# Kernel tuning notes

Measured on AMD Instinct MI355X. Metric: run time of the kernel, lower is better.

Reference implementation:

```python
import jax, jax.numpy as jnp
from jax import lax
import numpy as np

NPOINT = 1024
NSAMPLE = 32
BN_EPS = 1e-3  # Keras BatchNormalization default epsilon


def farthest_point_sample(xyz, npoint):
    # xyz: [B, N, 3] -> indices [B, npoint] (int32), sequential O(npoint*N)
    B, N, _ = xyz.shape

    def step(carry, _):
        distance, farthest = carry                                   # [B,N], [B]
        centroid = jnp.take_along_axis(xyz, farthest[:, None, None], axis=1)  # [B,1,3]
        dist = jnp.sum((xyz - centroid) ** 2, axis=-1)               # [B,N]
        distance = jnp.minimum(distance, dist)
        new_farthest = jnp.argmax(distance, axis=1).astype(jnp.int32)
        return (distance, new_farthest), farthest

    init = (jnp.full((B, N), 1e10, xyz.dtype), jnp.zeros((B,), jnp.int32))
    _, idxs = lax.scan(step, init, xs=None, length=npoint)           # [npoint, B]
    return jnp.transpose(idxs)                                       # [B, npoint]


def index_points_2d(points, idx):
    # points: [B,N,C], idx: [B,S] -> [B,S,C]
    return jnp.take_along_axis(points, idx[:, :, None], axis=1)


def index_points_3d(points, idx):
    # points: [B,N,C], idx: [B,S,K] -> [B,S,K,C]
    return jax.vmap(lambda p, i: p[i])(points, idx)


def query_ball_point(nsample, xyz, new_xyz):
    # nearest-nsample variant (radius is ignored, matching the source)
    # sq_dist: [B, S, N]
    sq = jnp.sum(new_xyz ** 2, axis=-1, keepdims=True) \
         - 2.0 * jnp.einsum('bsc,bnc->bsn', new_xyz, xyz) \
         + jnp.sum(xyz ** 2, axis=-1)[:, None, :]
    _, group_idx = lax.top_k(-sq, nsample)                           # [B,S,K]
    return group_idx


def bn_relu(x, g, b, mm, mv):
    # inference-mode BatchNorm (moving stats) + ReLU, per-channel on last dim
    return jax.nn.relu((x - mm) * lax.rsqrt(mv + BN_EPS) * g + b)


def setup_inputs() -> dict:
    key = jax.random.key(0)
    ks = jax.random.split(key, 20)
    B, N, D = 4, 16384, 64
    mlp = [64, 64, 128]
    cin = 3 + D  # 67
    inp = {
        'xyz': jax.random.normal(ks[0], (B, N, 3), jnp.float32),
        'points': jax.random.normal(ks[1], (B, N, D), jnp.float32),
    }
    c = cin
    for i, co in enumerate(mlp):
        inp[f'w{i}'] = jax.random.normal(ks[2 + 4 * i], (c, co), jnp.float32) * (1.0 / np.sqrt(c))
        inp[f'g{i}'] = jnp.ones((co,), jnp.float32)
        inp[f'b{i}'] = jnp.zeros((co,), jnp.float32)
        inp[f'mm{i}'] = jax.random.normal(ks[3 + 4 * i], (co,), jnp.float32) * 0.1
        inp[f'mv{i}'] = jax.random.uniform(ks[4 + 4 * i], (co,), jnp.float32, 0.5, 1.5)
        c = co
    return inp


def reference(xyz, points, w0, g0, b0, mm0, mv0, w1, g1, b1, mm1, mv1, w2, g2, b2, mm2, mv2):
    fps_idx = farthest_point_sample(xyz, NPOINT)                     # [B,S]
    new_xyz = index_points_2d(xyz, fps_idx)                          # [B,S,3]
    idx = query_ball_point(NSAMPLE, xyz, new_xyz)                    # [B,S,K]
    grouped_xyz = index_points_3d(xyz, idx)                          # [B,S,K,3]
    grouped_xyz_norm = grouped_xyz - new_xyz[:, :, None, :]
    grouped_points = index_points_3d(points, idx)                    # [B,S,K,D]
    x = jnp.concatenate([grouped_xyz_norm, grouped_points], axis=-1) # [B,S,K,3+D]
    for w, g, b, mm, mv in ((w0, g0, b0, mm0, mv0), (w1, g1, b1, mm1, mv1), (w2, g2, b2, mm2, mv2)):
        x = bn_relu(jnp.einsum('bskc,co->bsko', x, w), g, b, mm, mv)
    new_points = jnp.max(x, axis=2)                                  # [B,S,C_out]
    return (new_xyz, new_points)
```

## Files before the change

### kernel.cpp

```cpp
#include <hip/hip_runtime.h>
#include <hip/hip_bf16.h>
#include <stdint.h>

#define N_PTS 16384
#define S_OUT 1024


__global__ __launch_bounds__(512) void fps_kernel(
    const float* __restrict__ xyz,
    float* __restrict__ out_newxyz)
{
  const int b    = blockIdx.x;
  const int tid  = threadIdx.x;
  const int lane = tid & 63;
  const int wid  = tid >> 6;
  const float* base = xyz + (size_t)b * N_PTS * 3;

  float px[32], py[32], pz[32], dist[32];
#pragma unroll
  for (int i = 0; i < 32; ++i) {
    int n = tid * 32 + i;
    px[i] = base[n * 3 + 0];
    py[i] = base[n * 3 + 1];
    pz[i] = base[n * 3 + 2];
    dist[i] = 1e10f;
  }

  __shared__ float s_cx, s_cy, s_cz;
  __shared__ unsigned long long sred[8];

  if (tid == 0) { s_cx = px[0]; s_cy = py[0]; s_cz = pz[0]; }
  __syncthreads();

  for (int s = 0; s < S_OUT; ++s) {
    const float cx = s_cx, cy = s_cy, cz = s_cz;
    if (tid == 0) {
      size_t o = ((size_t)b * S_OUT + s) * 3;
      out_newxyz[o + 0] = cx;
      out_newxyz[o + 1] = cy;
      out_newxyz[o + 2] = cz;
    }
    unsigned long long best = 0ull;
#pragma unroll
    for (int i = 0; i < 32; ++i) {
      float dx = __fsub_rn(px[i], cx);
      float dy = __fsub_rn(py[i], cy);
      float dz = __fsub_rn(pz[i], cz);
      float dd = __fadd_rn(__fadd_rn(__fmul_rn(dx, dx), __fmul_rn(dy, dy)),
                           __fmul_rn(dz, dz));
      float dm = fminf(dist[i], dd);
      dist[i] = dm;
      unsigned long long key =
          ((unsigned long long)__float_as_uint(dm) << 32) |
          (unsigned long long)(0xFFFFFFFFu - (unsigned)(tid * 32 + i));
      if (key > best) best = key;
    }
#pragma unroll
    for (int off = 1; off < 64; off <<= 1) {
      unsigned long long o = __shfl_xor(best, off);
      if (o > best) best = o;
    }
    if (lane == 0) sred[wid] = best;
    __syncthreads();
    if (tid == 0) {
      unsigned long long m = sred[0];
#pragma unroll
      for (int w = 1; w < 8; ++w) if (sred[w] > m) m = sred[w];
      unsigned n = 0xFFFFFFFFu - (unsigned)(m & 0xFFFFFFFFull);
      const float* p = base + (size_t)n * 3;
      s_cx = p[0]; s_cy = p[1]; s_cz = p[2];
    }
    __syncthreads();
  }
}

__global__ __launch_bounds__(256, 2) void knn_kernel(
    const float* __restrict__ xyz,
    const float* __restrict__ newxyz,
    int* __restrict__ knn_out)
{
  const int bs  = blockIdx.x;
  const int b   = bs >> 10;
  const int tid = threadIdx.x;
  const float* base = xyz + (size_t)b * N_PTS * 3;

  const float qx = newxyz[(size_t)bs * 3 + 0];
  const float qy = newxyz[(size_t)bs * 3 + 1];
  const float qz = newxyz[(size_t)bs * 3 + 2];
  const float sumq = __fadd_rn(__fadd_rn(__fmul_rn(qx, qx), __fmul_rn(qy, qy)),
                               __fmul_rn(qz, qz));

  __shared__ unsigned hist[2048];
  __shared__ unsigned tsum[256];
  __shared__ unsigned long long cand[512];
  __shared__ unsigned long long s_min;
  __shared__ int s_b1, s_r1, s_b2, s_r2, s_cntL, s_cntC;

  for (int i = tid; i < 2048; i += 256) hist[i] = 0;
  if (tid == 0) { s_cntL = 0; s_cntC = 0; }
  __syncthreads();

#define KNN_KEY(n, u)                                                          \
    float x = base[(n) * 3 + 0];                                               \
    float y = base[(n) * 3 + 1];                                               \
    float z = base[(n) * 3 + 2];                                               \
    float sumx = __fadd_rn(__fadd_rn(__fmul_rn(x, x), __fmul_rn(y, y)),        \
                           __fmul_rn(z, z));                                   \
    float dot  = __fmul_rn(qx, x);                                             \
    dot = fmaf(qy, y, dot);                                                    \
    dot = fmaf(qz, z, dot);                                                    \
    float sq   = __fsub_rn(__fadd_rn(sumq, sumx), __fmul_rn(2.0f, dot));       \
    unsigned u = __float_as_uint(sq);                                          \
    u ^= (u & 0x80000000u) ? 0xFFFFFFFFu : 0x80000000u;

  for (int j = 0; j < 64; ++j) {
    int n = j * 256 + tid;
    KNN_KEY(n, u)
    atomicAdd(&hist[u >> 21], 1u);
  }
  __syncthreads();

  unsigned ts = 0;
#pragma unroll
  for (int u = 0; u < 8; ++u) ts += hist[tid * 8 + u];
  tsum[tid] = ts;
  __syncthreads();

  if (tid == 0) {
    unsigned acc = 0; int t2 = 0;
    for (; t2 < 256; ++t2) { unsigned h = tsum[t2]; if (acc + h >= 32u) break; acc += h; }
    int u2 = t2 * 8;
    for (;; ++u2) { unsigned h = hist[u2]; if (acc + h >= 32u) break; acc += h; }
    s_b1 = u2; s_r1 = 32 - (int)acc;
  }
  __syncthreads();
  const unsigned b1 = (unsigned)s_b1;
  const int r1 = s_r1;

  for (int i = tid; i < 2048; i += 256) hist[i] = 0;
  __syncthreads();

  for (int j = 0; j < 64; ++j) {
    int n = j * 256 + tid;
    KNN_KEY(n, u)
    if ((u >> 21) == b1) atomicAdd(&hist[(u >> 10) & 0x7FFu], 1u);
  }
  __syncthreads();

  ts = 0;
#pragma unroll
  for (int u = 0; u < 8; ++u) ts += hist[tid * 8 + u];
  tsum[tid] = ts;
  __syncthreads();

  if (tid == 0) {
    unsigned acc = 0; int t2 = 0;
    for (; t2 < 256; ++t2) { unsigned h = tsum[t2]; if (acc + h >= (unsigned)r1) break; acc += h; }
    int u2 = t2 * 8;
    for (;; ++u2) { unsigned h = hist[u2]; if (acc + h >= (unsigned)r1) break; acc += h; }
    s_b2 = u2; s_r2 = r1 - (int)acc;
  }
  __syncthreads();
  const unsigned b2 = (unsigned)s_b2;

  int* outp = knn_out + (size_t)bs * 32;

  for (int j = 0; j < 64; ++j) {
    int n = j * 256 + tid;
    KNN_KEY(n, u)
    unsigned bin = u >> 21;
    if (bin < b1) {
      int p = atomicAdd(&s_cntL, 1);
      outp[p] = n;
    } else if (bin == b1) {
      unsigned sub = (u >> 10) & 0x7FFu;
      if (sub < b2) {
        int p = atomicAdd(&s_cntL, 1);
        outp[p] = n;
      } else if (sub == b2) {
        int p = atomicAdd(&s_cntC, 1);
        if (p < 512) cand[p] = ((unsigned long long)u << 32) | (unsigned)n;
      }
    }
  }
  __syncthreads();
#undef KNN_KEY

  const int r   = s_r2;
  const int cl  = s_cntL;
  const int cnt = min(s_cntC, 512);
  unsigned long long last = 0ull;
  for (int i = 0; i < r; ++i) {
    if (tid == 0) s_min = ~0ull;
    __syncthreads();
    for (int p = tid; p < cnt; p += 256) {
      unsigned long long v = cand[p];
      if (i == 0 ? 1 : (v > last)) atomicMin(&s_min, v);
    }
    __syncthreads();
    unsigned long long m = s_min;
    if (tid == 0) outp[cl + i] = (int)(unsigned)(m & 0xFFFFFFFFull);
    last = m;
    __syncthreads();
  }
}

__global__ __launch_bounds__(256, 2) void mlp_kernel(
    const float* __restrict__ xyz,
    const float* __restrict__ points,
    const float* __restrict__ newxyz,
    const int* __restrict__ knn,
    const float* __restrict__ w0, const float* __restrict__ g0,
    const float* __restrict__ b0, const float* __restrict__ mm0,
    const float* __restrict__ mv0,
    const float* __restrict__ w1, const float* __restrict__ g1,
    const float* __restrict__ b1_, const float* __restrict__ mm1,
    const float* __restrict__ mv1,
    const float* __restrict__ w2, const float* __restrict__ g2,
    const float* __restrict__ b2_, const float* __restrict__ mm2,
    const float* __restrict__ mv2,
    float* __restrict__ out1)
{
  const int tid = threadIdx.x;
  const int BS0 = blockIdx.x * 2;

  __shared__ __align__(16) float xT[2][67][36];
  __shared__ __align__(16) float a1[2][64][36];
  __shared__ __align__(16) float wbuf[8192];

  {
    const int sg = tid >> 7;
    const int j  = (tid >> 2) & 31;
    const int cq = tid & 3;
    const int S  = BS0 + sg;
    const int bb = S >> 10;
    const int n  = knn[(size_t)S * 32 + j] & (N_PTS - 1);
    const float* pbase = points + ((size_t)bb * N_PTS + n) * 64;
    const float* xbase = xyz + ((size_t)bb * N_PTS + n) * 3;
    for (int c = cq; c < 67; c += 4) {
      float v;
      if (c < 3) v = __fsub_rn(xbase[c], newxyz[(size_t)S * 3 + c]);
      else       v = pbase[c - 3];
      xT[sg][c][j] = v;
    }
  }
  for (int i = tid; i < 67 * 64; i += 256) wbuf[i] = w0[i];
  __syncthreads();

  const int sg = tid >> 7;
  const int t  = tid & 127;

  {
    const int ot = t & 15, kt = t >> 4;
    const int o0 = ot * 4, k0 = kt * 4;
    float acc[4][4] = {};
    for (int c = 0; c < 67; ++c) {
      float4 xv = *(const float4*)&xT[sg][c][k0];
      float4 wq = *(const float4*)&wbuf[c * 64 + o0];
      float wv[4] = { wq.x, wq.y, wq.z, wq.w };
      float xs[4] = { xv.x, xv.y, xv.z, xv.w };
#pragma unroll
      for (int a = 0; a < 4; ++a)
#pragma unroll
        for (int k2 = 0; k2 < 4; ++k2)
          acc[a][k2] = fmaf(wv[a], xs[k2], acc[a][k2]);
    }
#pragma unroll
    for (int jj = 0; jj < 4; ++jj) {
      int o = o0 + jj;
      float A  = rsqrtf(mv0[o] + 1e-3f) * g0[o];
      float Bc = b0[o] - mm0[o] * A;
      float4 y;
      y.x = fmaxf(fmaf(acc[jj][0], A, Bc), 0.0f);
      y.y = fmaxf(fmaf(acc[jj][1], A, Bc), 0.0f);
      y.z = fmaxf(fmaf(acc[jj][2], A, Bc), 0.0f);
      y.w = fmaxf(fmaf(acc[jj][3], A, Bc), 0.0f);
      *(float4*)&a1[sg][o][k0] = y;
    }
  }
  __syncthreads();
  for (int i = tid; i < 64 * 64; i += 256) wbuf[i] = w1[i];
  __syncthreads();

  {
    const int ot = t & 15, kt = t >> 4;
    const int o0 = ot * 4, k0 = kt * 4;
    float acc[4][4] = {};
    for (int c = 0; c < 64; ++c) {
      float4 xv = *(const float4*)&a1[sg][c][k0];
      float4 wq = *(const float4*)&wbuf[c * 64 + o0];
      float wv[4] = { wq.x, wq.y, wq.z, wq.w };
      float xs[4] = { xv.x, xv.y, xv.z, xv.w };
#pragma unroll
      for (int a = 0; a < 4; ++a)
#pragma unroll
        for (int k2 = 0; k2 < 4; ++k2)
          acc[a][k2] = fmaf(wv[a], xs[k2], acc[a][k2]);
    }
#pragma unroll
    for (int jj = 0; jj < 4; ++jj) {
      int o = o0 + jj;
      float A  = rsqrtf(mv1[o] + 1e-3f) * g1[o];
      float Bc = b1_[o] - mm1[o] * A;
      float4 y;
      y.x = fmaxf(fmaf(acc[jj][0], A, Bc), 0.0f);
      y.y = fmaxf(fmaf(acc[jj][1], A, Bc), 0.0f);
      y.z = fmaxf(fmaf(acc[jj][2], A, Bc), 0.0f);
      y.w = fmaxf(fmaf(acc[jj][3], A, Bc), 0.0f);
      *(float4*)&xT[sg][o][k0] = y;
    }
  }
  __syncthreads();
  for (int i = tid; i < 64 * 128; i += 256) wbuf[i] = w2[i];
  __syncthreads();

  float* pm = &a1[0][0][0];
  {
    const int ot = t & 31, kt = t >> 5;
    const int o0 = ot * 4, k0 = kt * 8;
    float acc[4][8] = {};
    for (int c = 0; c < 64; ++c) {
      float4 xa = *(const float4*)&xT[sg][c][k0];
      float4 xb = *(const float4*)&xT[sg][c][k0 + 4];
      float4 wq = *(const float4*)&wbuf[c * 128 + o0];
      float wv[4] = { wq.x, wq.y, wq.z, wq.w };
      float xs[8] = { xa.x, xa.y, xa.z, xa.w, xb.x, xb.y, xb.z, xb.w };
#pragma unroll
      for (int a = 0; a < 4; ++a)
#pragma unroll
        for (int k2 = 0; k2 < 8; ++k2)
          acc[a][k2] = fmaf(wv[a], xs[k2], acc[a][k2]);
    }
#pragma unroll
    for (int jj = 0; jj < 4; ++jj) {
      int o = o0 + jj;
      float A  = rsqrtf(mv2[o] + 1e-3f) * g2[o];
      float Bc = b2_[o] - mm2[o] * A;
      float m = 0.0f;
#pragma unroll
      for (int kk = 0; kk < 8; ++kk)
        m = fmaxf(m, fmaf(acc[jj][kk], A, Bc));
      pm[((sg * 128 + o) << 2) + kt] = m;
    }
  }
  __syncthreads();
  {
    const int sg2 = tid >> 7, o = tid & 127;
    const int basep = (sg2 * 128 + o) << 2;
    float m = fmaxf(fmaxf(pm[basep + 0], pm[basep + 1]),
                    fmaxf(pm[basep + 2], pm[basep + 3]));
    out1[(size_t)(BS0 + sg2) * 128 + o] = m;
  }
}

extern "C" void kernel_launch(void* const* d_in, const int* in_sizes, int n_in,
                              void* d_out, int out_size, void* d_ws, size_t ws_size,
                              hipStream_t stream) {
  const float* xyz    = (const float*)d_in[0];
  const float* points = (const float*)d_in[1];
  const float* w0  = (const float*)d_in[2];
  const float* g0  = (const float*)d_in[3];
  const float* b0  = (const float*)d_in[4];
  const float* mm0 = (const float*)d_in[5];
  const float* mv0 = (const float*)d_in[6];
  const float* w1  = (const float*)d_in[7];
  const float* g1  = (const float*)d_in[8];
  const float* b1  = (const float*)d_in[9];
  const float* mm1 = (const float*)d_in[10];
  const float* mv1 = (const float*)d_in[11];
  const float* w2  = (const float*)d_in[12];
  const float* g2  = (const float*)d_in[13];
  const float* b2  = (const float*)d_in[14];
  const float* mm2 = (const float*)d_in[15];
  const float* mv2 = (const float*)d_in[16];

  float* out      = (float*)d_out;
  float* out_pts  = out + (size_t)4 * 1024 * 3;
  int*   knn      = (int*)d_ws;

  fps_kernel<<<4, 512, 0, stream>>>(xyz, out);
  knn_kernel<<<4096, 256, 0, stream>>>(xyz, out, knn);
  mlp_kernel<<<2048, 256, 0, stream>>>(xyz, points, out, knn,
      w0, g0, b0, mm0, mv0, w1, g1, b1, mm1, mv1, w2, g2, b2, mm2, mv2,
      out_pts);
}
```

Before: 2.099 ms.

## Streamline FPS argmax reduction with float shuffles and one barrier per step

The per-point argmax now keeps a float max plus a local index instead of building 64-bit keys. The wavefront reduction shuffles only the 32-bit float, then uses a ballot to find the winning lane's index. A double-buffered shared array lets every thread reduce the 8 per-wave results itself, which removes the second __syncthreads and the serial thread-0 centroid load per iteration. Launch bounds also request 2 blocks per CU. The cost is a redundant global load of the centroid by every thread, plus extra register pressure from the occupancy hint, which could cause spills of the 128 per-thread registers.

```diff
diff --git a/kernel.cpp b/kernel.cpp
--- a/kernel.cpp
+++ b/kernel.cpp
@@ -6,7 +6,7 @@
 #define S_OUT 1024
 
 
-__global__ __launch_bounds__(512) void fps_kernel(
+__global__ __launch_bounds__(512, 2) void fps_kernel(
     const float* __restrict__ xyz,
     float* __restrict__ out_newxyz)
 {
@@ -26,21 +26,21 @@
     dist[i] = 1e10f;
   }
 
-  __shared__ float s_cx, s_cy, s_cz;
-  __shared__ unsigned long long sred[8];
-
-  if (tid == 0) { s_cx = px[0]; s_cy = py[0]; s_cz = pz[0]; }
-  __syncthreads();
+  __shared__ unsigned long long sred[2][8];
+
+  float cx = base[0], cy = base[1], cz = base[2];
 
   for (int s = 0; s < S_OUT; ++s) {
-    const float cx = s_cx, cy = s_cy, cz = s_cz;
     if (tid == 0) {
       size_t o = ((size_t)b * S_OUT + s) * 3;
       out_newxyz[o + 0] = cx;
       out_newxyz[o + 1] = cy;
       out_newxyz[o + 2] = cz;
     }
-    unsigned long long best = 0ull;
+    if (s == S_OUT - 1) break;
+
+    float best  = -1.0f;
+    int   bestI = 0;
 #pragma unroll
     for (int i = 0; i < 32; ++i) {
       float dx = __fsub_rn(px[i], cx);
@@ -50,27 +50,36 @@
                            __fmul_rn(dz, dz));
       float dm = fminf(dist[i], dd);
       dist[i] = dm;
-      unsigned long long key =
-          ((unsigned long long)__float_as_uint(dm) << 32) |
-          (unsigned long long)(0xFFFFFFFFu - (unsigned)(tid * 32 + i));
-      if (key > best) best = key;
-    }
-#pragma unroll
-    for (int off = 1; off < 64; off <<= 1) {
-      unsigned long long o = __shfl_xor(best, off);
-      if (o > best) best = o;
-    }
-    if (lane == 0) sred[wid] = best;
+      bool c = dm > best;
+      best  = c ? dm : best;
+      bestI = c ? i  : bestI;
+    }
+    const unsigned bestN = (unsigned)(tid * 32 + bestI);
+
+    float m = best;
+#pragma unroll
+    for (int off = 1; off < 64; off <<= 1)
+      m = fmaxf(m, __shfl_xor(m, off));
+    unsigned long long msk = __ballot(best == m);
+    int wl = __ffsll(msk) - 1;
+    unsigned wn = (unsigned)__shfl((int)bestN, wl);
+
+    const int p = s & 1;
+    if (lane == 0)
+      sred[p][wid] = ((unsigned long long)__float_as_uint(m) << 32) |
+                     (unsigned long long)(0xFFFFFFFFu - wn);
     __syncthreads();
-    if (tid == 0) {
-      unsigned long long m = sred[0];
-#pragma unroll
-      for (int w = 1; w < 8; ++w) if (sred[w] > m) m = sred[w];
-      unsigned n = 0xFFFFFFFFu - (unsigned)(m & 0xFFFFFFFFull);
-      const float* p = base + (size_t)n * 3;
-      s_cx = p[0]; s_cy = p[1]; s_cz = p[2];
-    }
-    __syncthreads();
+
+    unsigned long long k = sred[p][0];
+#pragma unroll
+    for (int w = 1; w < 8; ++w) {
+      unsigned long long v = sred[p][w];
+      if (v > k) k = v;
+    }
+    unsigned n = 0xFFFFFFFFu - (unsigned)(k & 0xFFFFFFFFull);
+    n = __builtin_amdgcn_readfirstlane(n);
+    const float* pc = base + (size_t)n * 3;
+    cx = pc[0]; cy = pc[1]; cz = pc[2];
   }
 }
 
```

Result: slower. 2.153 ms (+2.6%).
